# Kernel tuning notes

Measured on AMD Instinct MI355X. Metric: run time of the kernel, lower is better.

The kernel has to match this reference:

```python
import jax, jax.numpy as jnp
import numpy as np

N_NODES = 50000
N_EDGES = 800000
D_IN = 64
F1 = 64
F2 = 64
D_HID = 100


def setup_inputs() -> dict:
    key = jax.random.key(0)
    ks = jax.random.split(key, 12)
    x = jax.random.normal(ks[0], (N_NODES, D_IN), dtype=jnp.float32)
    edge_src = jax.random.randint(ks[1], (N_EDGES,), 0, N_NODES, dtype=jnp.int32)
    edge_dst = jax.random.randint(ks[2], (N_EDGES,), 0, N_NODES, dtype=jnp.int32)
    # stands in for pre-normalized GCN adjacency values (D^-1/2 (A+I) D^-1/2)
    edge_weight = jax.random.uniform(ks[3], (N_EDGES,), dtype=jnp.float32)
    def glorot(k, shape):
        lim = np.sqrt(6.0 / (shape[0] + shape[1]))
        return jax.random.uniform(k, shape, jnp.float32, -lim, lim)
    W1 = glorot(ks[4], (D_IN, F1))
    b1 = jnp.zeros((F1,), jnp.float32)
    W2 = glorot(ks[5], (F1, F2))
    b2 = jnp.zeros((F2,), jnp.float32)
    Wd = glorot(ks[6], (F2, D_HID))
    bd = jnp.zeros((D_HID,), jnp.float32)
    Wo = glorot(ks[7], (D_HID, 1))
    bo = jnp.zeros((1,), jnp.float32)
    return {"x": x, "edge_src": edge_src, "edge_dst": edge_dst,
            "edge_weight": edge_weight, "W1": W1, "b1": b1, "W2": W2,
            "b2": b2, "Wd": Wd, "bd": bd, "Wo": Wo, "bo": bo}


def _gcn_conv(x, edge_src, edge_dst, edge_weight, W, b):
    # spektral GCNConv: out = swish(A_norm @ (X @ W) + b)
    h = x @ W                                        # [N, F]
    msg = h[edge_src] * edge_weight[:, None]          # [E, F] gather + scale
    agg = jax.ops.segment_sum(msg, edge_dst, num_segments=N_NODES)  # [N, F]
    return jax.nn.swish(agg + b)


def reference(x, edge_src, edge_dst, edge_weight, W1, b1, W2, b2, Wd, bd, Wo, bo):
    h = _gcn_conv(x, edge_src, edge_dst, edge_weight, W1, b1)
    h = _gcn_conv(h, edge_src, edge_dst, edge_weight, W2, b2)
    h = jax.nn.swish(h @ Wd + bd)                    # Dense(100, swish)
    return jax.nn.sigmoid(h @ Wo + bo)               # Dense(1, sigmoid) -> [N, 1]
```

## Files before the change

kernel.cpp:

```cpp
#include <hip/hip_runtime.h>
#include <hip/hip_fp16.h>

#define N_NODES 50000
#define N_EDGES 800000
#define D 64
#define DHID 100
#define NTILES (N_NODES / 16)
#define NCT 7
#define CAP 64
#define NGROUPS 8
#define NSLICES 390
#define FILL_BLOCKS (NGROUPS * NSLICES)
#define MM_BLOCKS ((NTILES + 3) / 4)
#define DST_PER_GROUP (N_NODES / NGROUPS)

typedef unsigned short ushort;
typedef unsigned int uint;
typedef __attribute__((ext_vector_type(8))) short s16x8;
typedef __attribute__((ext_vector_type(4))) float f32x4;

#define MFMA16(A, B, C) __builtin_amdgcn_mfma_f32_16x16x32_bf16((A), (B), (C), 0, 0, 0)

__device__ __forceinline__ float swishf(float x) { return x / (1.0f + __expf(-x)); }

__device__ __forceinline__ ushort f2bf(float f) {
    uint u = __float_as_uint(f);
    uint r = (u + 0x7fffu + ((u >> 16) & 1u)) >> 16;
    return (ushort)r;
}
__device__ __forceinline__ float bf2f(ushort h) { return __uint_as_float((uint)h << 16); }
__device__ __forceinline__ float bf_lo(uint d) { return __uint_as_float(d << 16); }
__device__ __forceinline__ float bf_hi(uint d) { return __uint_as_float(d & 0xffff0000u); }

__device__ __forceinline__ float hwf(uint e) {
    return __half2float(__ushort_as_half((ushort)(e >> 16)));
}

__device__ __forceinline__ void accum8(float* acc, uint4 v, float w) {
    acc[0] = fmaf(w, bf_lo(v.x), acc[0]);
    acc[1] = fmaf(w, bf_hi(v.x), acc[1]);
    acc[2] = fmaf(w, bf_lo(v.y), acc[2]);
    acc[3] = fmaf(w, bf_hi(v.y), acc[3]);
    acc[4] = fmaf(w, bf_lo(v.z), acc[4]);
    acc[5] = fmaf(w, bf_hi(v.z), acc[5]);
    acc[6] = fmaf(w, bf_lo(v.w), acc[6]);
    acc[7] = fmaf(w, bf_hi(v.w), acc[7]);
}

__global__ __launch_bounds__(256) void fill_and_l1(const int* __restrict__ src,
                                                   const int* __restrict__ dst,
                                                   const float* __restrict__ w,
                                                   int* __restrict__ deg,
                                                   uint* __restrict__ csr,
                                                   const float* __restrict__ X,
                                                   const float* __restrict__ W,
                                                   ushort* __restrict__ H) {
    __shared__ __align__(16) short sBT[2][D][72];
    __shared__ __align__(16) short rep[4][16][72];
    int tid = threadIdx.x;

    if (blockIdx.x < FILL_BLOCKS) {
        const int g = blockIdx.x & (NGROUPS - 1);
        const int s = blockIdx.x >> 3;
        const int lo = g * DST_PER_GROUP;
        const int hi = lo + DST_PER_GROUP;
        for (int e = s * 256 + tid; e < N_EDGES; e += NSLICES * 256) {
            int d = dst[e];
            if (d >= lo && d < hi) {
                uint hw = (uint)__half_as_ushort(__float2half_rn(w[e]));
                uint payload = (uint)src[e] | (hw << 16);
                int r = atomicAdd(&deg[d], 1);
                r = min(r, CAP - 1);
                csr[(d << 6) + r] = payload;
            }
        }
        return;
    }

    for (int idx = tid; idx < D * D; idx += 256) {
        int k = idx >> 6, c = idx & 63;
        float wv = W[idx];
        ushort hi = f2bf(wv);
        sBT[0][c][k] = (short)hi;
        sBT[1][c][k] = (short)f2bf(wv - bf2f(hi));
    }
    __syncthreads();
    int wv_ = tid >> 6, lane = tid & 63, quad = lane >> 4, m = lane & 15;
    int tile = (blockIdx.x - FILL_BLOCKS) * 4 + wv_;
    if (tile >= NTILES) return;
    int node0 = tile * 16;

    f32x4 acc[4] = {{0,0,0,0},{0,0,0,0},{0,0,0,0},{0,0,0,0}};
#pragma unroll
    for (int kt = 0; kt < 2; ++kt) {
        int k0 = kt * 32 + quad * 8;
        const float* xp = X + ((size_t)(node0 + m) << 6) + k0;
        float4 xa = *((const float4*)xp);
        float4 xb = *((const float4*)(xp + 4));
        float xv[8] = {xa.x, xa.y, xa.z, xa.w, xb.x, xb.y, xb.z, xb.w};
        s16x8 ahi, alo;
#pragma unroll
        for (int jj = 0; jj < 8; ++jj) {
            ushort hi = f2bf(xv[jj]);
            ahi[jj] = (short)hi;
            alo[jj] = (short)f2bf(xv[jj] - bf2f(hi));
        }
#pragma unroll
        for (int ct = 0; ct < 4; ++ct) {
            int n = ct * 16 + m;
            s16x8 bhi = *((const s16x8*)&sBT[0][n][k0]);
            s16x8 blo = *((const s16x8*)&sBT[1][n][k0]);
            acc[ct] = MFMA16(ahi, bhi, acc[ct]);
            acc[ct] = MFMA16(ahi, blo, acc[ct]);
            acc[ct] = MFMA16(alo, bhi, acc[ct]);
        }
    }
#pragma unroll
    for (int ct = 0; ct < 4; ++ct)
#pragma unroll
        for (int r = 0; r < 4; ++r)
            rep[wv_][quad * 4 + r][ct * 16 + m] = (short)f2bf(acc[ct][r]);
#pragma unroll
    for (int half = 0; half < 2; ++half) {
        int r = (lane >> 3) + half * 8;
        int c0 = (lane & 7) * 8;
        s16x8 v = *((const s16x8*)&rep[wv_][r][c0]);
        *((s16x8*)(H + ((size_t)(node0 + r) << 6) + c0)) = v;
    }
}

__global__ __launch_bounds__(256) void mfma_l2(const ushort* __restrict__ act,
                                               const float* __restrict__ W,
                                               ushort* __restrict__ H) {
    __shared__ __align__(16) short sBT[2][D][72];
    __shared__ __align__(16) short rep[4][16][72];
    int tid = threadIdx.x;
    for (int idx = tid; idx < D * D; idx += 256) {
        int k = idx >> 6, c = idx & 63;
        float wv = W[idx];
        ushort hi = f2bf(wv);
        sBT[0][c][k] = (short)hi;
        sBT[1][c][k] = (short)f2bf(wv - bf2f(hi));
    }
    __syncthreads();
    int w = tid >> 6, lane = tid & 63, quad = lane >> 4, m = lane & 15;
    int tile = blockIdx.x * 4 + w;
    if (tile >= NTILES) return;
    int node0 = tile * 16;

    f32x4 acc[4] = {{0,0,0,0},{0,0,0,0},{0,0,0,0},{0,0,0,0}};
#pragma unroll
    for (int kt = 0; kt < 2; ++kt) {
        int k0 = kt * 32 + quad * 8;
        s16x8 a = *((const s16x8*)(act + ((size_t)(node0 + m) << 6) + k0));
#pragma unroll
        for (int ct = 0; ct < 4; ++ct) {
            int n = ct * 16 + m;
            s16x8 bhi = *((const s16x8*)&sBT[0][n][k0]);
            s16x8 blo = *((const s16x8*)&sBT[1][n][k0]);
            acc[ct] = MFMA16(a, bhi, acc[ct]);
            acc[ct] = MFMA16(a, blo, acc[ct]);
        }
    }
#pragma unroll
    for (int ct = 0; ct < 4; ++ct)
#pragma unroll
        for (int r = 0; r < 4; ++r)
            rep[w][quad * 4 + r][ct * 16 + m] = (short)f2bf(acc[ct][r]);
#pragma unroll
    for (int half = 0; half < 2; ++half) {
        int r = (lane >> 3) + half * 8;
        int c0 = (lane & 7) * 8;
        s16x8 v = *((const s16x8*)&rep[w][r][c0]);
        *((s16x8*)(H + ((size_t)(node0 + r) << 6) + c0)) = v;
    }
}

__global__ __launch_bounds__(256) void gather_act(const ushort* __restrict__ H,
                                                  const int* __restrict__ deg,
                                                  const uint* __restrict__ csr,
                                                  const float* __restrict__ bias,
                                                  ushort* __restrict__ actOut) {
    int tid = threadIdx.x;
    int wave = tid >> 6, lane = tid & 63;
    int j = lane >> 3, fg = lane & 7;
    int node = blockIdx.x * 4 + wave;
    int degv = min(deg[node], CAP);
    const uint* bucket = csr + ((size_t)node << 6);

    float acc[8] = {0, 0, 0, 0, 0, 0, 0, 0};
    if (degv > 16) {
        int last = degv - 1;
        for (int base = 0; base < degv; base += 32) {
            int i0 = base + j, i1 = i0 + 8, i2 = i0 + 16, i3 = i0 + 24;
            uint e0 = bucket[min(i0, last)];
            uint e1 = bucket[min(i1, last)];
            uint e2 = bucket[min(i2, last)];
            uint e3 = bucket[min(i3, last)];
            float w0 = (i0 <= last) ? hwf(e0) : 0.f;
            float w1 = (i1 <= last) ? hwf(e1) : 0.f;
            float w2 = (i2 <= last) ? hwf(e2) : 0.f;
            float w3 = (i3 <= last) ? hwf(e3) : 0.f;
            uint4 v0 = *((const uint4*)(H + ((size_t)(e0 & 0xffffu) << 6) + (fg << 3)));
            uint4 v1 = *((const uint4*)(H + ((size_t)(e1 & 0xffffu) << 6) + (fg << 3)));
            uint4 v2 = *((const uint4*)(H + ((size_t)(e2 & 0xffffu) << 6) + (fg << 3)));
            uint4 v3 = *((const uint4*)(H + ((size_t)(e3 & 0xffffu) << 6) + (fg << 3)));
            accum8(acc, v0, w0);
            accum8(acc, v1, w1);
            accum8(acc, v2, w2);
            accum8(acc, v3, w3);
        }
    } else if (degv > 0) {
        int last = degv - 1;
        int i1 = j + 8;
        uint e0 = bucket[min(j, last)];
        uint e1 = bucket[min(i1, last)];
        float w0 = (j <= last) ? hwf(e0) : 0.f;
        float w1 = (i1 <= last) ? hwf(e1) : 0.f;
        uint4 v0 = *((const uint4*)(H + ((size_t)(e0 & 0xffffu) << 6) + (fg << 3)));
        uint4 v1 = *((const uint4*)(H + ((size_t)(e1 & 0xffffu) << 6) + (fg << 3)));
        accum8(acc, v0, w0);
        accum8(acc, v1, w1);
    }
#pragma unroll
    for (int t = 0; t < 8; ++t) {
        acc[t] += __shfl_xor(acc[t], 8, 64);
        acc[t] += __shfl_xor(acc[t], 16, 64);
        acc[t] += __shfl_xor(acc[t], 32, 64);
    }
    if (j == 0) {
        float4 ba = ((const float4*)bias)[fg * 2];
        float4 bb = ((const float4*)bias)[fg * 2 + 1];
        float r0 = swishf(acc[0] + ba.x);
        float r1 = swishf(acc[1] + ba.y);
        float r2 = swishf(acc[2] + ba.z);
        float r3 = swishf(acc[3] + ba.w);
        float r4 = swishf(acc[4] + bb.x);
        float r5 = swishf(acc[5] + bb.y);
        float r6 = swishf(acc[6] + bb.z);
        float r7 = swishf(acc[7] + bb.w);
        uint4 u;
        u.x = (uint)f2bf(r0) | ((uint)f2bf(r1) << 16);
        u.y = (uint)f2bf(r2) | ((uint)f2bf(r3) << 16);
        u.z = (uint)f2bf(r4) | ((uint)f2bf(r5) << 16);
        u.w = (uint)f2bf(r6) | ((uint)f2bf(r7) << 16);
        *((uint4*)(actOut + ((size_t)node << 6) + (fg << 3))) = u;
    }
}

__global__ __launch_bounds__(256) void mfma_head(const ushort* __restrict__ act2,
                                                 const float* __restrict__ Wd,
                                                 const float* __restrict__ bd,
                                                 const float* __restrict__ Wo,
                                                 const float* __restrict__ bo,
                                                 float* __restrict__ out) {
    __shared__ __align__(16) short sBT[2][NCT * 16][72];
    __shared__ float sbd[NCT * 16];
    __shared__ float sWo[NCT * 16];
    int tid = threadIdx.x;
    for (int idx = tid; idx < NCT * 16 * D; idx += 256) {
        int jj = idx >> 6, k = idx & 63;
        float wv = (jj < DHID) ? Wd[k * DHID + jj] : 0.f;
        ushort hi = f2bf(wv);
        sBT[0][jj][k] = (short)hi;
        sBT[1][jj][k] = (short)f2bf(wv - bf2f(hi));
    }
    if (tid < NCT * 16) {
        sbd[tid] = (tid < DHID) ? bd[tid] : 0.f;
        sWo[tid] = (tid < DHID) ? Wo[tid] : 0.f;
    }
    __syncthreads();
    int w = tid >> 6, lane = tid & 63, quad = lane >> 4, m = lane & 15;
    int tile = blockIdx.x * 4 + w;
    if (tile >= NTILES) return;
    int node0 = tile * 16;

    f32x4 acc[NCT];
#pragma unroll
    for (int ct = 0; ct < NCT; ++ct) acc[ct] = (f32x4){0, 0, 0, 0};
#pragma unroll
    for (int kt = 0; kt < 2; ++kt) {
        int k0 = kt * 32 + quad * 8;
        s16x8 a = *((const s16x8*)(act2 + ((size_t)(node0 + m) << 6) + k0));
#pragma unroll
        for (int ct = 0; ct < NCT; ++ct) {
            int n = ct * 16 + m;
            s16x8 bhi = *((const s16x8*)&sBT[0][n][k0]);
            s16x8 blo = *((const s16x8*)&sBT[1][n][k0]);
            acc[ct] = MFMA16(a, bhi, acc[ct]);
            acc[ct] = MFMA16(a, blo, acc[ct]);
        }
    }
    float part[4] = {0, 0, 0, 0};
#pragma unroll
    for (int ct = 0; ct < NCT; ++ct) {
        int jj = ct * 16 + m;
        float bdv = sbd[jj], wov = sWo[jj];
#pragma unroll
        for (int r = 0; r < 4; ++r)
            part[r] = fmaf(swishf(acc[ct][r] + bdv), wov, part[r]);
    }
#pragma unroll
    for (int r = 0; r < 4; ++r) {
        part[r] += __shfl_xor(part[r], 1, 64);
        part[r] += __shfl_xor(part[r], 2, 64);
        part[r] += __shfl_xor(part[r], 4, 64);
        part[r] += __shfl_xor(part[r], 8, 64);
    }
    if (m == 0) {
        float b0 = bo[0];
        float4 o;
        o.x = 1.f / (1.f + __expf(-(part[0] + b0)));
        o.y = 1.f / (1.f + __expf(-(part[1] + b0)));
        o.z = 1.f / (1.f + __expf(-(part[2] + b0)));
        o.w = 1.f / (1.f + __expf(-(part[3] + b0)));
        *((float4*)(out + node0 + quad * 4)) = o;
    }
}

extern "C" void kernel_launch(void* const* d_in, const int* in_sizes, int n_in,
                              void* d_out, int out_size, void* d_ws, size_t ws_size,
                              hipStream_t stream) {
    const float* x   = (const float*)d_in[0];
    const int* esrc  = (const int*)d_in[1];
    const int* edst  = (const int*)d_in[2];
    const float* ew  = (const float*)d_in[3];
    const float* W1  = (const float*)d_in[4];
    const float* b1  = (const float*)d_in[5];
    const float* W2  = (const float*)d_in[6];
    const float* b2  = (const float*)d_in[7];
    const float* Wd  = (const float*)d_in[8];
    const float* bd  = (const float*)d_in[9];
    const float* Wo  = (const float*)d_in[10];
    const float* bo  = (const float*)d_in[11];
    float* out = (float*)d_out;

    char* ws = (char*)d_ws;
    ushort* H1   = (ushort*)ws;  ws += (size_t)N_NODES * D * sizeof(ushort);
    ushort* act1 = (ushort*)ws;  ws += (size_t)N_NODES * D * sizeof(ushort);
    ushort* H2   = (ushort*)ws;  ws += (size_t)N_NODES * D * sizeof(ushort);
    ushort* act2 = (ushort*)ws;  ws += (size_t)N_NODES * D * sizeof(ushort);
    uint* csr    = (uint*)ws;    ws += (size_t)N_NODES * CAP * sizeof(uint);
    int* deg     = (int*)ws;     ws += (size_t)N_NODES * sizeof(int);

    const int gBlocks = N_NODES / 4;

    hipMemsetAsync(deg, 0, (size_t)N_NODES * sizeof(int), stream);

    fill_and_l1<<<FILL_BLOCKS + MM_BLOCKS, 256, 0, stream>>>(esrc, edst, ew, deg, csr,
                                                             x, W1, H1);

    gather_act<<<gBlocks, 256, 0, stream>>>(H1, deg, csr, b1, act1);

    mfma_l2<<<(NTILES + 3) / 4, 256, 0, stream>>>(act1, W2, H2);
    gather_act<<<gBlocks, 256, 0, stream>>>(H2, deg, csr, b2, act2);

    mfma_head<<<(NTILES + 3) / 4, 256, 0, stream>>>(act2, Wd, bd, Wo, bo, out);
}
```

Before: 199.7 us.

## Reorder layer-2 as aggregate-then-transform and fuse W2 matmul into head kernel

Uses associativity A(XW) = (AX)W for the second GCN layer. It gathers act1 directly into an fp32 aggregate, then multiplies by W2 inside the head kernel and keeps the swish activation in shared memory. This removes the mfma_l2 kernel launch and the H2/act2 bf16 global round trips. In exchange, the aggregate is written in fp32 (twice the bytes) and the head kernel gains a split-precision 3-MFMA stage. Layer 1 now reuses the weight shared buffer for output staging and clamps out-of-range tiles instead of returning early.

```diff
diff --git a/kernel.cpp b/kernel.cpp
--- a/kernel.cpp
+++ b/kernel.cpp
@@ -56,7 +56,6 @@
                                                    const float* __restrict__ W,
                                                    ushort* __restrict__ H) {
     __shared__ __align__(16) short sBT[2][D][72];
-    __shared__ __align__(16) short rep[4][16][72];
     int tid = threadIdx.x;
 
     if (blockIdx.x < FILL_BLOCKS) {
@@ -86,8 +85,7 @@
     }
     __syncthreads();
     int wv_ = tid >> 6, lane = tid & 63, quad = lane >> 4, m = lane & 15;
-    int tile = (blockIdx.x - FILL_BLOCKS) * 4 + wv_;
-    if (tile >= NTILES) return;
+    int tile = min((blockIdx.x - FILL_BLOCKS) * 4 + wv_, NTILES - 1);
     int node0 = tile * 16;
 
     f32x4 acc[4] = {{0,0,0,0},{0,0,0,0},{0,0,0,0},{0,0,0,0}};
@@ -115,6 +113,8 @@
             acc[ct] = MFMA16(alo, bhi, acc[ct]);
         }
     }
+    __syncthreads();
+    short (*rep)[16][72] = (short(*)[16][72])&sBT[0][0][0];
 #pragma unroll
     for (int ct = 0; ct < 4; ++ct)
 #pragma unroll
@@ -125,53 +125,6 @@
         int r = (lane >> 3) + half * 8;
         int c0 = (lane & 7) * 8;
         s16x8 v = *((const s16x8*)&rep[wv_][r][c0]);
-        *((s16x8*)(H + ((size_t)(node0 + r) << 6) + c0)) = v;
-    }
-}
-
-__global__ __launch_bounds__(256) void mfma_l2(const ushort* __restrict__ act,
-                                               const float* __restrict__ W,
-                                               ushort* __restrict__ H) {
-    __shared__ __align__(16) short sBT[2][D][72];
-    __shared__ __align__(16) short rep[4][16][72];
-    int tid = threadIdx.x;
-    for (int idx = tid; idx < D * D; idx += 256) {
-        int k = idx >> 6, c = idx & 63;
-        float wv = W[idx];
-        ushort hi = f2bf(wv);
-        sBT[0][c][k] = (short)hi;
-        sBT[1][c][k] = (short)f2bf(wv - bf2f(hi));
-    }
-    __syncthreads();
-    int w = tid >> 6, lane = tid & 63, quad = lane >> 4, m = lane & 15;
-    int tile = blockIdx.x * 4 + w;
-    if (tile >= NTILES) return;
-    int node0 = tile * 16;
-
-    f32x4 acc[4] = {{0,0,0,0},{0,0,0,0},{0,0,0,0},{0,0,0,0}};
-#pragma unroll
-    for (int kt = 0; kt < 2; ++kt) {
-        int k0 = kt * 32 + quad * 8;
-        s16x8 a = *((const s16x8*)(act + ((size_t)(node0 + m) << 6) + k0));
-#pragma unroll
-        for (int ct = 0; ct < 4; ++ct) {
-            int n = ct * 16 + m;
-            s16x8 bhi = *((const s16x8*)&sBT[0][n][k0]);
-            s16x8 blo = *((const s16x8*)&sBT[1][n][k0]);
-            acc[ct] = MFMA16(a, bhi, acc[ct]);
-            acc[ct] = MFMA16(a, blo, acc[ct]);
-        }
-    }
-#pragma unroll
-    for (int ct = 0; ct < 4; ++ct)
-#pragma unroll
-        for (int r = 0; r < 4; ++r)
-            rep[w][quad * 4 + r][ct * 16 + m] = (short)f2bf(acc[ct][r]);
-#pragma unroll
-    for (int half = 0; half < 2; ++half) {
-        int r = (lane >> 3) + half * 8;
-        int c0 = (lane & 7) * 8;
-        s16x8 v = *((const s16x8*)&rep[w][r][c0]);
         *((s16x8*)(H + ((size_t)(node0 + r) << 6) + c0)) = v;
     }
 }
@@ -248,16 +201,132 @@
     }
 }
 
-__global__ __launch_bounds__(256) void mfma_head(const ushort* __restrict__ act2,
+__global__ __launch_bounds__(256) void gather_raw(const ushort* __restrict__ H,
+                                                  const int* __restrict__ deg,
+                                                  const uint* __restrict__ csr,
+                                                  float* __restrict__ aggOut) {
+    int tid = threadIdx.x;
+    int wave = tid >> 6, lane = tid & 63;
+    int j = lane >> 3, fg = lane & 7;
+    int node = blockIdx.x * 4 + wave;
+    int degv = min(deg[node], CAP);
+    const uint* bucket = csr + ((size_t)node << 6);
+
+    float acc[8] = {0, 0, 0, 0, 0, 0, 0, 0};
+    if (degv > 16) {
+        int last = degv - 1;
+        for (int base = 0; base < degv; base += 32) {
+            int i0 = base + j, i1 = i0 + 8, i2 = i0 + 16, i3 = i0 + 24;
+            uint e0 = bucket[min(i0, last)];
+            uint e1 = bucket[min(i1, last)];
+            uint e2 = bucket[min(i2, last)];
+            uint e3 = bucket[min(i3, last)];
+            float w0 = (i0 <= last) ? hwf(e0) : 0.f;
+            float w1 = (i1 <= last) ? hwf(e1) : 0.f;
+            float w2 = (i2 <= last) ? hwf(e2) : 0.f;
+            float w3 = (i3 <= last) ? hwf(e3) : 0.f;
+            uint4 v0 = *((const uint4*)(H + ((size_t)(e0 & 0xffffu) << 6) + (fg << 3)));
+            uint4 v1 = *((const uint4*)(H + ((size_t)(e1 & 0xffffu) << 6) + (fg << 3)));
+            uint4 v2 = *((const uint4*)(H + ((size_t)(e2 & 0xffffu) << 6) + (fg << 3)));
+            uint4 v3 = *((const uint4*)(H + ((size_t)(e3 & 0xffffu) << 6) + (fg << 3)));
+            accum8(acc, v0, w0);
+            accum8(acc, v1, w1);
+            accum8(acc, v2, w2);
+            accum8(acc, v3, w3);
+        }
+    } else if (degv > 0) {
+        int last = degv - 1;
+        int i1 = j + 8;
+        uint e0 = bucket[min(j, last)];
+        uint e1 = bucket[min(i1, last)];
+        float w0 = (j <= last) ? hwf(e0) : 0.f;
+        float w1 = (i1 <= last) ? hwf(e1) : 0.f;
+        uint4 v0 = *((const uint4*)(H + ((size_t)(e0 & 0xffffu) << 6) + (fg << 3)));
+        uint4 v1 = *((const uint4*)(H + ((size_t)(e1 & 0xffffu) << 6) + (fg << 3)));
+        accum8(acc, v0, w0);
+        accum8(acc, v1, w1);
+    }
+#pragma unroll
+    for (int t = 0; t < 8; ++t) {
+        acc[t] += __shfl_xor(acc[t], 8, 64);
+        acc[t] += __shfl_xor(acc[t], 16, 64);
+        acc[t] += __shfl_xor(acc[t], 32, 64);
+    }
+    if (j == 0) {
+        float4 u0 = {acc[0], acc[1], acc[2], acc[3]};
+        float4 u1 = {acc[4], acc[5], acc[6], acc[7]};
+        float* p = aggOut + ((size_t)node << 6) + (fg << 3);
+        *((float4*)p) = u0;
+        *((float4*)(p + 4)) = u1;
+    }
+}
+
+__global__ __launch_bounds__(256) void mfma_tail(const float* __restrict__ agg2,
+                                                 const float* __restrict__ W2,
+                                                 const float* __restrict__ b2,
                                                  const float* __restrict__ Wd,
                                                  const float* __restrict__ bd,
                                                  const float* __restrict__ Wo,
                                                  const float* __restrict__ bo,
                                                  float* __restrict__ out) {
     __shared__ __align__(16) short sBT[2][NCT * 16][72];
+    __shared__ __align__(16) short sAct[4][16][72];
+    __shared__ float sb2[D];
     __shared__ float sbd[NCT * 16];
     __shared__ float sWo[NCT * 16];
     int tid = threadIdx.x;
+
+    for (int idx = tid; idx < D * D; idx += 256) {
+        int k = idx >> 6, c = idx & 63;
+        float wv = W2[idx];
+        ushort hi = f2bf(wv);
+        sBT[0][c][k] = (short)hi;
+        sBT[1][c][k] = (short)f2bf(wv - bf2f(hi));
+    }
+    if (tid < D) sb2[tid] = b2[tid];
+    __syncthreads();
+
+    int w = tid >> 6, lane = tid & 63, quad = lane >> 4, m = lane & 15;
+    int tile = min(blockIdx.x * 4 + w, NTILES - 1);
+    int node0 = tile * 16;
+
+    {
+        f32x4 acc[4] = {{0,0,0,0},{0,0,0,0},{0,0,0,0},{0,0,0,0}};
+#pragma unroll
+        for (int kt = 0; kt < 2; ++kt) {
+            int k0 = kt * 32 + quad * 8;
+            const float* ap = agg2 + ((size_t)(node0 + m) << 6) + k0;
+            float4 xa = *((const float4*)ap);
+            float4 xb = *((const float4*)(ap + 4));
+            float xv[8] = {xa.x, xa.y, xa.z, xa.w, xb.x, xb.y, xb.z, xb.w};
+            s16x8 ahi, alo;
+#pragma unroll
+            for (int jj = 0; jj < 8; ++jj) {
+                ushort hi = f2bf(xv[jj]);
+                ahi[jj] = (short)hi;
+                alo[jj] = (short)f2bf(xv[jj] - bf2f(hi));
+            }
+#pragma unroll
+            for (int ct = 0; ct < 4; ++ct) {
+                int n = ct * 16 + m;
+                s16x8 bhi = *((const s16x8*)&sBT[0][n][k0]);
+                s16x8 blo = *((const s16x8*)&sBT[1][n][k0]);
+                acc[ct] = MFMA16(ahi, bhi, acc[ct]);
+                acc[ct] = MFMA16(ahi, blo, acc[ct]);
+                acc[ct] = MFMA16(alo, bhi, acc[ct]);
+            }
+        }
+#pragma unroll
+        for (int ct = 0; ct < 4; ++ct) {
+            int col = ct * 16 + m;
+            float bv = sb2[col];
+#pragma unroll
+            for (int r = 0; r < 4; ++r)
+                sAct[w][quad * 4 + r][col] = (short)f2bf(swishf(acc[ct][r] + bv));
+        }
+    }
+    __syncthreads();
+
     for (int idx = tid; idx < NCT * 16 * D; idx += 256) {
         int jj = idx >> 6, k = idx & 63;
         float wv = (jj < DHID) ? Wd[k * DHID + jj] : 0.f;
@@ -270,10 +339,6 @@
         sWo[tid] = (tid < DHID) ? Wo[tid] : 0.f;
     }
     __syncthreads();
-    int w = tid >> 6, lane = tid & 63, quad = lane >> 4, m = lane & 15;
-    int tile = blockIdx.x * 4 + w;
-    if (tile >= NTILES) return;
-    int node0 = tile * 16;
 
     f32x4 acc[NCT];
 #pragma unroll
@@ -281,7 +346,7 @@
 #pragma unroll
     for (int kt = 0; kt < 2; ++kt) {
         int k0 = kt * 32 + quad * 8;
-        s16x8 a = *((const s16x8*)(act2 + ((size_t)(node0 + m) << 6) + k0));
+        s16x8 a = *((const s16x8*)&sAct[w][m][k0]);
 #pragma unroll
         for (int ct = 0; ct < NCT; ++ct) {
             int n = ct * 16 + m;
@@ -338,8 +403,7 @@
     char* ws = (char*)d_ws;
     ushort* H1   = (ushort*)ws;  ws += (size_t)N_NODES * D * sizeof(ushort);
     ushort* act1 = (ushort*)ws;  ws += (size_t)N_NODES * D * sizeof(ushort);
-    ushort* H2   = (ushort*)ws;  ws += (size_t)N_NODES * D * sizeof(ushort);
-    ushort* act2 = (ushort*)ws;  ws += (size_t)N_NODES * D * sizeof(ushort);
+    float*  agg2 = (float*)ws;   ws += (size_t)N_NODES * D * sizeof(float);
     uint* csr    = (uint*)ws;    ws += (size_t)N_NODES * CAP * sizeof(uint);
     int* deg     = (int*)ws;     ws += (size_t)N_NODES * sizeof(int);
 
@@ -352,8 +416,7 @@
 
     gather_act<<<gBlocks, 256, 0, stream>>>(H1, deg, csr, b1, act1);
 
-    mfma_l2<<<(NTILES + 3) / 4, 256, 0, stream>>>(act1, W2, H2);
-    gather_act<<<gBlocks, 256, 0, stream>>>(H2, deg, csr, b2, act2);
-
-    mfma_head<<<(NTILES + 3) / 4, 256, 0, stream>>>(act2, Wd, bd, Wo, bo, out);
-}
+    gather_raw<<<gBlocks, 256, 0, stream>>>(act1, deg, csr, agg2);
+
+    mfma_tail<<<MM_BLOCKS, 256, 0, stream>>>(agg2, W2, b2, Wd, bd, Wo, bo, out);
+}
```

After: 198.3 us. About the same (-0.7%).

## Aggregate before transform in layer 2 and fuse with dense head

Applied to the files above, without the earlier changes.

Uses associativity, A(XW) = (AX)W, to gather act1 rows first, then apply W2, swish, the Wd/Wo head and the sigmoid all inside one kernel per 16-node tile. This removes the H2/act2 round trips and two kernel launches. W2 and Wd are pre-split into hi/lo bf16 pairs by extra blocks in the first kernel, and edge loads are made nontemporal. In exchange the gather kernel now does per-block MFMA work with extra syncthreads, and the second-layer weights are read from global memory instead of LDS.

```diff
diff --git a/kernel.cpp b/kernel.cpp
--- a/kernel.cpp
+++ b/kernel.cpp
@@ -47,148 +47,11 @@
     acc[7] = fmaf(w, bf_hi(v.w), acc[7]);
 }
 
-__global__ __launch_bounds__(256) void fill_and_l1(const int* __restrict__ src,
-                                                   const int* __restrict__ dst,
-                                                   const float* __restrict__ w,
-                                                   int* __restrict__ deg,
-                                                   uint* __restrict__ csr,
-                                                   const float* __restrict__ X,
-                                                   const float* __restrict__ W,
-                                                   ushort* __restrict__ H) {
-    __shared__ __align__(16) short sBT[2][D][72];
-    __shared__ __align__(16) short rep[4][16][72];
-    int tid = threadIdx.x;
-
-    if (blockIdx.x < FILL_BLOCKS) {
-        const int g = blockIdx.x & (NGROUPS - 1);
-        const int s = blockIdx.x >> 3;
-        const int lo = g * DST_PER_GROUP;
-        const int hi = lo + DST_PER_GROUP;
-        for (int e = s * 256 + tid; e < N_EDGES; e += NSLICES * 256) {
-            int d = dst[e];
-            if (d >= lo && d < hi) {
-                uint hw = (uint)__half_as_ushort(__float2half_rn(w[e]));
-                uint payload = (uint)src[e] | (hw << 16);
-                int r = atomicAdd(&deg[d], 1);
-                r = min(r, CAP - 1);
-                csr[(d << 6) + r] = payload;
-            }
-        }
-        return;
-    }
-
-    for (int idx = tid; idx < D * D; idx += 256) {
-        int k = idx >> 6, c = idx & 63;
-        float wv = W[idx];
-        ushort hi = f2bf(wv);
-        sBT[0][c][k] = (short)hi;
-        sBT[1][c][k] = (short)f2bf(wv - bf2f(hi));
-    }
-    __syncthreads();
-    int wv_ = tid >> 6, lane = tid & 63, quad = lane >> 4, m = lane & 15;
-    int tile = (blockIdx.x - FILL_BLOCKS) * 4 + wv_;
-    if (tile >= NTILES) return;
-    int node0 = tile * 16;
-
-    f32x4 acc[4] = {{0,0,0,0},{0,0,0,0},{0,0,0,0},{0,0,0,0}};
-#pragma unroll
-    for (int kt = 0; kt < 2; ++kt) {
-        int k0 = kt * 32 + quad * 8;
-        const float* xp = X + ((size_t)(node0 + m) << 6) + k0;
-        float4 xa = *((const float4*)xp);
-        float4 xb = *((const float4*)(xp + 4));
-        float xv[8] = {xa.x, xa.y, xa.z, xa.w, xb.x, xb.y, xb.z, xb.w};
-        s16x8 ahi, alo;
-#pragma unroll
-        for (int jj = 0; jj < 8; ++jj) {
-            ushort hi = f2bf(xv[jj]);
-            ahi[jj] = (short)hi;
-            alo[jj] = (short)f2bf(xv[jj] - bf2f(hi));
-        }
-#pragma unroll
-        for (int ct = 0; ct < 4; ++ct) {
-            int n = ct * 16 + m;
-            s16x8 bhi = *((const s16x8*)&sBT[0][n][k0]);
-            s16x8 blo = *((const s16x8*)&sBT[1][n][k0]);
-            acc[ct] = MFMA16(ahi, bhi, acc[ct]);
-            acc[ct] = MFMA16(ahi, blo, acc[ct]);
-            acc[ct] = MFMA16(alo, bhi, acc[ct]);
-        }
-    }
-#pragma unroll
-    for (int ct = 0; ct < 4; ++ct)
-#pragma unroll
-        for (int r = 0; r < 4; ++r)
-            rep[wv_][quad * 4 + r][ct * 16 + m] = (short)f2bf(acc[ct][r]);
-#pragma unroll
-    for (int half = 0; half < 2; ++half) {
-        int r = (lane >> 3) + half * 8;
-        int c0 = (lane & 7) * 8;
-        s16x8 v = *((const s16x8*)&rep[wv_][r][c0]);
-        *((s16x8*)(H + ((size_t)(node0 + r) << 6) + c0)) = v;
-    }
-}
-
-__global__ __launch_bounds__(256) void mfma_l2(const ushort* __restrict__ act,
-                                               const float* __restrict__ W,
-                                               ushort* __restrict__ H) {
-    __shared__ __align__(16) short sBT[2][D][72];
-    __shared__ __align__(16) short rep[4][16][72];
-    int tid = threadIdx.x;
-    for (int idx = tid; idx < D * D; idx += 256) {
-        int k = idx >> 6, c = idx & 63;
-        float wv = W[idx];
-        ushort hi = f2bf(wv);
-        sBT[0][c][k] = (short)hi;
-        sBT[1][c][k] = (short)f2bf(wv - bf2f(hi));
-    }
-    __syncthreads();
-    int w = tid >> 6, lane = tid & 63, quad = lane >> 4, m = lane & 15;
-    int tile = blockIdx.x * 4 + w;
-    if (tile >= NTILES) return;
-    int node0 = tile * 16;
-
-    f32x4 acc[4] = {{0,0,0,0},{0,0,0,0},{0,0,0,0},{0,0,0,0}};
-#pragma unroll
-    for (int kt = 0; kt < 2; ++kt) {
-        int k0 = kt * 32 + quad * 8;
-        s16x8 a = *((const s16x8*)(act + ((size_t)(node0 + m) << 6) + k0));
-#pragma unroll
-        for (int ct = 0; ct < 4; ++ct) {
-            int n = ct * 16 + m;
-            s16x8 bhi = *((const s16x8*)&sBT[0][n][k0]);
-            s16x8 blo = *((const s16x8*)&sBT[1][n][k0]);
-            acc[ct] = MFMA16(a, bhi, acc[ct]);
-            acc[ct] = MFMA16(a, blo, acc[ct]);
-        }
-    }
-#pragma unroll
-    for (int ct = 0; ct < 4; ++ct)
-#pragma unroll
-        for (int r = 0; r < 4; ++r)
-            rep[w][quad * 4 + r][ct * 16 + m] = (short)f2bf(acc[ct][r]);
-#pragma unroll
-    for (int half = 0; half < 2; ++half) {
-        int r = (lane >> 3) + half * 8;
-        int c0 = (lane & 7) * 8;
-        s16x8 v = *((const s16x8*)&rep[w][r][c0]);
-        *((s16x8*)(H + ((size_t)(node0 + r) << 6) + c0)) = v;
-    }
-}
-
-__global__ __launch_bounds__(256) void gather_act(const ushort* __restrict__ H,
-                                                  const int* __restrict__ deg,
-                                                  const uint* __restrict__ csr,
-                                                  const float* __restrict__ bias,
-                                                  ushort* __restrict__ actOut) {
-    int tid = threadIdx.x;
-    int wave = tid >> 6, lane = tid & 63;
-    int j = lane >> 3, fg = lane & 7;
-    int node = blockIdx.x * 4 + wave;
-    int degv = min(deg[node], CAP);
-    const uint* bucket = csr + ((size_t)node << 6);
-
-    float acc[8] = {0, 0, 0, 0, 0, 0, 0, 0};
+__device__ __forceinline__ void gather_node(const ushort* __restrict__ H,
+                                            const uint* __restrict__ bucket,
+                                            int degv, int j, int fg, float* acc) {
+#pragma unroll
+    for (int t = 0; t < 8; ++t) acc[t] = 0.f;
     if (degv > 16) {
         int last = degv - 1;
         for (int base = 0; base < degv; base += 32) {
@@ -228,6 +91,131 @@
         acc[t] += __shfl_xor(acc[t], 16, 64);
         acc[t] += __shfl_xor(acc[t], 32, 64);
     }
+}
+
+__global__ __launch_bounds__(256) void fill_and_l1(const int* __restrict__ src,
+                                                   const int* __restrict__ dst,
+                                                   const float* __restrict__ w,
+                                                   int* __restrict__ deg,
+                                                   uint* __restrict__ csr,
+                                                   const float* __restrict__ X,
+                                                   const float* __restrict__ W,
+                                                   const float* __restrict__ W2,
+                                                   const float* __restrict__ Wd,
+                                                   short* __restrict__ W2T2,
+                                                   short* __restrict__ WdT2,
+                                                   ushort* __restrict__ H) {
+    __shared__ __align__(16) short sBT[2][D][72];
+    int tid = threadIdx.x;
+
+    if (blockIdx.x < FILL_BLOCKS) {
+        const int g = blockIdx.x & (NGROUPS - 1);
+        const int s = blockIdx.x >> 3;
+        const int lo = g * DST_PER_GROUP;
+        const int hi = lo + DST_PER_GROUP;
+        for (int e = s * 256 + tid; e < N_EDGES; e += NSLICES * 256) {
+            int d = __builtin_nontemporal_load(&dst[e]);
+            if (d >= lo && d < hi) {
+                int sv = __builtin_nontemporal_load(&src[e]);
+                float wvv = __builtin_nontemporal_load(&w[e]);
+                uint hw = (uint)__half_as_ushort(__float2half_rn(wvv));
+                uint payload = (uint)sv | (hw << 16);
+                int r = atomicAdd(&deg[d], 1);
+                r = min(r, CAP - 1);
+                csr[(d << 6) + r] = payload;
+            }
+        }
+        return;
+    }
+
+    if (blockIdx.x >= FILL_BLOCKS + MM_BLOCKS) {
+        if (blockIdx.x == FILL_BLOCKS + MM_BLOCKS) {
+            for (int idx = tid; idx < D * D; idx += 256) {
+                int k = idx >> 6, c = idx & 63;
+                float wv = W2[idx];
+                ushort hi = f2bf(wv);
+                W2T2[(size_t)c * D + k] = (short)hi;
+                W2T2[(size_t)(D + c) * D + k] = (short)f2bf(wv - bf2f(hi));
+            }
+        } else {
+            for (int idx = tid; idx < NCT * 16 * D; idx += 256) {
+                int jj = idx >> 6, k = idx & 63;
+                float wv = (jj < DHID) ? Wd[k * DHID + jj] : 0.f;
+                ushort hi = f2bf(wv);
+                WdT2[(size_t)jj * D + k] = (short)hi;
+                WdT2[(size_t)(NCT * 16 + jj) * D + k] = (short)f2bf(wv - bf2f(hi));
+            }
+        }
+        return;
+    }
+
+    for (int idx = tid; idx < D * D; idx += 256) {
+        int k = idx >> 6, c = idx & 63;
+        float wv = W[idx];
+        ushort hi = f2bf(wv);
+        sBT[0][c][k] = (short)hi;
+        sBT[1][c][k] = (short)f2bf(wv - bf2f(hi));
+    }
+    __syncthreads();
+    int wv_ = tid >> 6, lane = tid & 63, quad = lane >> 4, m = lane & 15;
+    int tile = min((blockIdx.x - FILL_BLOCKS) * 4 + wv_, NTILES - 1);
+    int node0 = tile * 16;
+
+    f32x4 acc[4] = {{0,0,0,0},{0,0,0,0},{0,0,0,0},{0,0,0,0}};
+#pragma unroll
+    for (int kt = 0; kt < 2; ++kt) {
+        int k0 = kt * 32 + quad * 8;
+        const float* xp = X + ((size_t)(node0 + m) << 6) + k0;
+        float4 xa = *((const float4*)xp);
+        float4 xb = *((const float4*)(xp + 4));
+        float xv[8] = {xa.x, xa.y, xa.z, xa.w, xb.x, xb.y, xb.z, xb.w};
+        s16x8 ahi, alo;
+#pragma unroll
+        for (int jj = 0; jj < 8; ++jj) {
+            ushort hi = f2bf(xv[jj]);
+            ahi[jj] = (short)hi;
+            alo[jj] = (short)f2bf(xv[jj] - bf2f(hi));
+        }
+#pragma unroll
+        for (int ct = 0; ct < 4; ++ct) {
+            int n = ct * 16 + m;
+            s16x8 bhi = *((const s16x8*)&sBT[0][n][k0]);
+            s16x8 blo = *((const s16x8*)&sBT[1][n][k0]);
+            acc[ct] = MFMA16(ahi, bhi, acc[ct]);
+            acc[ct] = MFMA16(ahi, blo, acc[ct]);
+            acc[ct] = MFMA16(alo, bhi, acc[ct]);
+        }
+    }
+    __syncthreads();
+    short (*rep)[16][72] = (short(*)[16][72])&sBT[0][0][0];
+#pragma unroll
+    for (int ct = 0; ct < 4; ++ct)
+#pragma unroll
+        for (int r = 0; r < 4; ++r)
+            rep[wv_][quad * 4 + r][ct * 16 + m] = (short)f2bf(acc[ct][r]);
+#pragma unroll
+    for (int half = 0; half < 2; ++half) {
+        int r = (lane >> 3) + half * 8;
+        int c0 = (lane & 7) * 8;
+        s16x8 v = *((const s16x8*)&rep[wv_][r][c0]);
+        *((s16x8*)(H + ((size_t)(node0 + r) << 6) + c0)) = v;
+    }
+}
+
+__global__ __launch_bounds__(256) void gather_act(const ushort* __restrict__ H,
+                                                  const int* __restrict__ deg,
+                                                  const uint* __restrict__ csr,
+                                                  const float* __restrict__ bias,
+                                                  ushort* __restrict__ actOut) {
+    int tid = threadIdx.x;
+    int wave = tid >> 6, lane = tid & 63;
+    int j = lane >> 3, fg = lane & 7;
+    int node = blockIdx.x * 4 + wave;
+    int degv = min(deg[node], CAP);
+    const uint* bucket = csr + ((size_t)node << 6);
+
+    float acc[8];
+    gather_node(H, bucket, degv, j, fg, acc);
     if (j == 0) {
         float4 ba = ((const float4*)bias)[fg * 2];
         float4 bb = ((const float4*)bias)[fg * 2 + 1];
@@ -248,57 +236,92 @@
     }
 }
 
-__global__ __launch_bounds__(256) void mfma_head(const ushort* __restrict__ act2,
-                                                 const float* __restrict__ Wd,
-                                                 const float* __restrict__ bd,
-                                                 const float* __restrict__ Wo,
-                                                 const float* __restrict__ bo,
-                                                 float* __restrict__ out) {
-    __shared__ __align__(16) short sBT[2][NCT * 16][72];
-    __shared__ float sbd[NCT * 16];
-    __shared__ float sWo[NCT * 16];
+__global__ __launch_bounds__(256) void gather_tail(const ushort* __restrict__ act1,
+                                                   const int* __restrict__ deg,
+                                                   const uint* __restrict__ csr,
+                                                   const short* __restrict__ W2T2,
+                                                   const float* __restrict__ b2,
+                                                   const short* __restrict__ WdT2,
+                                                   const float* __restrict__ bd,
+                                                   const float* __restrict__ Wo,
+                                                   const float* __restrict__ bo,
+                                                   float* __restrict__ out) {
+    __shared__ __align__(16) float sAgg[16][72];
+    __shared__ __align__(16) short sAct2[16][72];
+    __shared__ float sPart[4][16];
     int tid = threadIdx.x;
-    for (int idx = tid; idx < NCT * 16 * D; idx += 256) {
-        int jj = idx >> 6, k = idx & 63;
-        float wv = (jj < DHID) ? Wd[k * DHID + jj] : 0.f;
-        ushort hi = f2bf(wv);
-        sBT[0][jj][k] = (short)hi;
-        sBT[1][jj][k] = (short)f2bf(wv - bf2f(hi));
-    }
-    if (tid < NCT * 16) {
-        sbd[tid] = (tid < DHID) ? bd[tid] : 0.f;
-        sWo[tid] = (tid < DHID) ? Wo[tid] : 0.f;
-    }
-    __syncthreads();
-    int w = tid >> 6, lane = tid & 63, quad = lane >> 4, m = lane & 15;
-    int tile = blockIdx.x * 4 + w;
-    if (tile >= NTILES) return;
-    int node0 = tile * 16;
-
-    f32x4 acc[NCT];
-#pragma unroll
-    for (int ct = 0; ct < NCT; ++ct) acc[ct] = (f32x4){0, 0, 0, 0};
-#pragma unroll
-    for (int kt = 0; kt < 2; ++kt) {
-        int k0 = kt * 32 + quad * 8;
-        s16x8 a = *((const s16x8*)(act2 + ((size_t)(node0 + m) << 6) + k0));
-#pragma unroll
-        for (int ct = 0; ct < NCT; ++ct) {
+    int wv = tid >> 6, lane = tid & 63;
+    int j = lane >> 3, fg = lane & 7;
+    int quad = lane >> 4, m = lane & 15;
+    int node0 = blockIdx.x * 16;
+
+    for (int t = 0; t < 4; ++t) {
+        int nl = wv * 4 + t;
+        int node = node0 + nl;
+        int degv = min(deg[node], CAP);
+        const uint* bucket = csr + ((size_t)node << 6);
+        float acc[8];
+        gather_node(act1, bucket, degv, j, fg, acc);
+        if (j == 0) {
+            float4 u0 = {acc[0], acc[1], acc[2], acc[3]};
+            float4 u1 = {acc[4], acc[5], acc[6], acc[7]};
+            *((float4*)&sAgg[nl][fg * 8]) = u0;
+            *((float4*)&sAgg[nl][fg * 8 + 4]) = u1;
+        }
+    }
+    __syncthreads();
+
+    {
+        f32x4 acc = {0, 0, 0, 0};
+        int n = wv * 16 + m;
+#pragma unroll
+        for (int kt = 0; kt < 2; ++kt) {
+            int k0 = kt * 32 + quad * 8;
+            float4 xa = *((const float4*)&sAgg[m][k0]);
+            float4 xb = *((const float4*)&sAgg[m][k0 + 4]);
+            float xv[8] = {xa.x, xa.y, xa.z, xa.w, xb.x, xb.y, xb.z, xb.w};
+            s16x8 ahi, alo;
+#pragma unroll
+            for (int jj = 0; jj < 8; ++jj) {
+                ushort hi = f2bf(xv[jj]);
+                ahi[jj] = (short)hi;
+                alo[jj] = (short)f2bf(xv[jj] - bf2f(hi));
+            }
+            s16x8 bhi = *((const s16x8*)(W2T2 + (size_t)n * D + k0));
+            s16x8 blo = *((const s16x8*)(W2T2 + (size_t)(D + n) * D + k0));
+            acc = MFMA16(ahi, bhi, acc);
+            acc = MFMA16(ahi, blo, acc);
+            acc = MFMA16(alo, bhi, acc);
+        }
+        float bv = b2[n];
+#pragma unroll
+        for (int r = 0; r < 4; ++r)
+            sAct2[quad * 4 + r][n] = (short)f2bf(swishf(acc[r] + bv));
+    }
+    __syncthreads();
+
+    float part[4] = {0, 0, 0, 0};
+#pragma unroll
+    for (int cc = 0; cc < 2; ++cc) {
+        int ct = wv + cc * 4;
+        if (ct < NCT) {
+            f32x4 acc = {0, 0, 0, 0};
             int n = ct * 16 + m;
-            s16x8 bhi = *((const s16x8*)&sBT[0][n][k0]);
-            s16x8 blo = *((const s16x8*)&sBT[1][n][k0]);
-            acc[ct] = MFMA16(a, bhi, acc[ct]);
-            acc[ct] = MFMA16(a, blo, acc[ct]);
-        }
-    }
-    float part[4] = {0, 0, 0, 0};
-#pragma unroll
-    for (int ct = 0; ct < NCT; ++ct) {
-        int jj = ct * 16 + m;
-        float bdv = sbd[jj], wov = sWo[jj];
-#pragma unroll
-        for (int r = 0; r < 4; ++r)
-            part[r] = fmaf(swishf(acc[ct][r] + bdv), wov, part[r]);
+#pragma unroll
+            for (int kt = 0; kt < 2; ++kt) {
+                int k0 = kt * 32 + quad * 8;
+                s16x8 a = *((const s16x8*)&sAct2[m][k0]);
+                s16x8 bhi = *((const s16x8*)(WdT2 + (size_t)n * D + k0));
+                s16x8 blo = *((const s16x8*)(WdT2 + (size_t)(NCT * 16 + n) * D + k0));
+                acc = MFMA16(a, bhi, acc);
+                acc = MFMA16(a, blo, acc);
+            }
+            float bdv = (n < DHID) ? bd[n] : 0.f;
+            float wov = (n < DHID) ? Wo[n] : 0.f;
+#pragma unroll
+            for (int r = 0; r < 4; ++r)
+                part[r] = fmaf(swishf(acc[r] + bdv), wov, part[r]);
+        }
     }
 #pragma unroll
     for (int r = 0; r < 4; ++r) {
@@ -308,13 +331,14 @@
         part[r] += __shfl_xor(part[r], 8, 64);
     }
     if (m == 0) {
-        float b0 = bo[0];
-        float4 o;
-        o.x = 1.f / (1.f + __expf(-(part[0] + b0)));
-        o.y = 1.f / (1.f + __expf(-(part[1] + b0)));
-        o.z = 1.f / (1.f + __expf(-(part[2] + b0)));
-        o.w = 1.f / (1.f + __expf(-(part[3] + b0)));
-        *((float4*)(out + node0 + quad * 4)) = o;
+#pragma unroll
+        for (int r = 0; r < 4; ++r)
+            sPart[wv][quad * 4 + r] = part[r];
+    }
+    __syncthreads();
+    if (tid < 16) {
+        float z = sPart[0][tid] + sPart[1][tid] + sPart[2][tid] + sPart[3][tid] + bo[0];
+        out[node0 + tid] = 1.f / (1.f + __expf(-z));
     }
 }
 
@@ -338,22 +362,19 @@
     char* ws = (char*)d_ws;
     ushort* H1   = (ushort*)ws;  ws += (size_t)N_NODES * D * sizeof(ushort);
     ushort* act1 = (ushort*)ws;  ws += (size_t)N_NODES * D * sizeof(ushort);
-    ushort* H2   = (ushort*)ws;  ws += (size_t)N_NODES * D * sizeof(ushort);
-    ushort* act2 = (ushort*)ws;  ws += (size_t)N_NODES * D * sizeof(ushort);
     uint* csr    = (uint*)ws;    ws += (size_t)N_NODES * CAP * sizeof(uint);
     int* deg     = (int*)ws;     ws += (size_t)N_NODES * sizeof(int);
+    short* W2T2  = (short*)ws;   ws += (size_t)2 * D * D * sizeof(short);
+    short* WdT2  = (short*)ws;   ws += (size_t)2 * NCT * 16 * D * sizeof(short);
 
     const int gBlocks = N_NODES / 4;
 
     hipMemsetAsync(deg, 0, (size_t)N_NODES * sizeof(int), stream);
 
-    fill_and_l1<<<FILL_BLOCKS + MM_BLOCKS, 256, 0, stream>>>(esrc, edst, ew, deg, csr,
-                                                             x, W1, H1);
+    fill_and_l1<<<FILL_BLOCKS + MM_BLOCKS + 2, 256, 0, stream>>>(
+        esrc, edst, ew, deg, csr, x, W1, W2, Wd, W2T2, WdT2, H1);
 
     gather_act<<<gBlocks, 256, 0, stream>>>(H1, deg, csr, b1, act1);
 
-    mfma_l2<<<(NTILES + 3) / 4, 256, 0, stream>>>(act1, W2, H2);
-    gather_act<<<gBlocks, 256, 0, stream>>>(H2, deg, csr, b2, act2);
-
-    mfma_head<<<(NTILES + 3) / 4, 256, 0, stream>>>(act2, Wd, bd, Wo, bo, out);
-}
+    gather_tail<<<NTILES, 256, 0, stream>>>(act1, deg, csr, W2T2, b2, WdT2, bd, Wo, bo, out);
+}
```

New measurement: 192.0 us. 3.9% less time.
